# Performance work log

Measured on AMD Instinct MI355X. Metric: run time of the kernel, lower is better.

Reference implementation:

```python
import jax, jax.numpy as jnp
import numpy as np

N = 50000        # nodes
E = 600000       # edges
D = 128          # hidden dim
FID = 128        # fixed_input_dim (one-hot size)
RWSE = 16        # rwse_dim
G = 128          # num graphs
L = 4            # num GIN blocks
DEG = 1001       # degree embedding table (clamp to 1000)
GIN_EPS = 0.0
BN_EPS = 1e-5


def setup_inputs() -> dict:
    key = jax.random.key(0)
    ks = jax.random.split(key, 16)
    s = 0.05
    inp = {
        "feat_id": jax.random.randint(ks[0], (N,), 0, 100000),
        "edge_index": jax.random.randint(ks[1], (2, E), 0, N),
        "batch_idx": jnp.sort(jax.random.randint(ks[2], (N,), 0, G)),
        "rwse": jax.random.normal(ks[3], (N, RWSE), jnp.float32),
        "in_degrees": jax.random.randint(ks[4], (N,), 0, DEG),
        # parameters
        "value_W": jax.random.normal(ks[5], (FID, D), jnp.float32) * s,
        "value_b": jnp.zeros((D,), jnp.float32),
        "rwse_W": jax.random.normal(ks[6], (RWSE, D), jnp.float32) * s,
        "rwse_b": jnp.zeros((D,), jnp.float32),
        "deg_emb": jax.random.normal(ks[7], (DEG, D), jnp.float32) * s,
        "mlp_W1": jax.random.normal(ks[8], (L, D, D), jnp.float32) * s,
        "mlp_b1": jnp.zeros((L, D), jnp.float32),
        "mlp_W2": jax.random.normal(ks[9], (L, D, D), jnp.float32) * s,
        "mlp_b2": jnp.zeros((L, D), jnp.float32),
        "bn_gamma": 1.0 + jax.random.normal(ks[10], (L, D), jnp.float32) * s,
        "bn_beta": jax.random.normal(ks[11], (L, D), jnp.float32) * s,
        "bn_mean": jax.random.normal(ks[12], (L, D), jnp.float32) * s,
        "bn_var": 1.0 + jax.random.uniform(ks[13], (L, D), jnp.float32) * 0.1,
    }
    return inp


def reference(feat_id, edge_index, batch_idx, rwse, in_degrees,
              value_W, value_b, rwse_W, rwse_b, deg_emb,
              mlp_W1, mlp_b1, mlp_W2, mlp_b2,
              bn_gamma, bn_beta, bn_mean, bn_var):
    # one_hot(feat_id % FID) @ value_W  ==  row gather of value_W
    h_id = jnp.remainder(feat_id, FID)
    h_attr = value_W[h_id] + value_b                      # [N, D]
    h_attr = h_attr + rwse @ rwse_W + rwse_b              # rwse projection
    deg = jnp.clip(in_degrees, 0, DEG - 1)
    h = h_attr + deg_emb[deg]                             # [N, D]

    src, dst = edge_index[0], edge_index[1]
    for l in range(L):
        # GIN aggregation: sum of neighbor messages + (1+eps)*self
        agg = jax.ops.segment_sum(h[src], dst, num_segments=N)
        agg = agg + (1.0 + GIN_EPS) * h
        # MLP: Linear -> ReLU -> Linear
        m = jax.nn.relu(agg @ mlp_W1[l] + mlp_b1[l]) @ mlp_W2[l] + mlp_b2[l]
        # BatchNorm (inference stats) + ReLU
        inv = bn_gamma[l] * jax.lax.rsqrt(bn_var[l] + BN_EPS)
        h = jax.nn.relu((m - bn_mean[l]) * inv + bn_beta[l])

    # scatter-mean graph pooling
    pooled = jax.ops.segment_sum(h, batch_idx, num_segments=G)      # [G, D]
    count = jax.ops.segment_sum(jnp.ones((N, 1), h.dtype), batch_idx,
                                num_segments=G)                     # [G, 1]
    graph_feature = pooled / jnp.maximum(count, 1.0)
    return graph_feature, h
```

## Files before the change

kernel.cpp:

```cpp
#include <hip/hip_runtime.h>

#define N_NODES 50000
#define N_EDGES 600000
#define DIM 128
#define NGRAPH 128
#define NLAYER 4
#define BN_EPS 1e-5f
#define SCAN_BLK 1024

using short8  = __attribute__((ext_vector_type(8))) short;
using float4v = __attribute__((ext_vector_type(4))) float;

__device__ __forceinline__ float bf2f(unsigned short u) {
    union { unsigned int i; float f; } c; c.i = ((unsigned int)u) << 16; return c.f;
}
__device__ __forceinline__ unsigned short f2bf(float f) {
    union { float f; unsigned int i; } c; c.f = f;
    unsigned int x = c.i;
    return (unsigned short)((x + 0x7fffu + ((x >> 16) & 1u)) >> 16);
}

__global__ void encode_kernel(const int* __restrict__ feat_id,
                              const float* __restrict__ rwse,
                              const int* __restrict__ indeg,
                              const float* __restrict__ value_W,
                              const float* __restrict__ value_b,
                              const float* __restrict__ rwse_W,
                              const float* __restrict__ rwse_b,
                              const float* __restrict__ deg_emb,
                              unsigned short* __restrict__ hout)
{
    int idx = blockIdx.x * blockDim.x + threadIdx.x;
    if (idx >= N_NODES * DIM) return;
    int n = idx >> 7, d = idx & 127;
    int fid = feat_id[n] & 127;
    float v = value_W[fid * DIM + d] + value_b[d] + rwse_b[d];
    const float* rr = rwse + n * 16;
    float acc = 0.f;
#pragma unroll
    for (int k = 0; k < 16; ++k) acc += rr[k] * rwse_W[k * DIM + d];
    v += acc;
    int dg = indeg[n]; dg = dg < 0 ? 0 : (dg > 1000 ? 1000 : dg);
    v += deg_emb[dg * DIM + d];
    hout[idx] = f2bf(v);
}

__global__ void hist_kernel(const int* __restrict__ dst, int* __restrict__ cnt) {
    int e = blockIdx.x * blockDim.x + threadIdx.x;
    if (e < N_EDGES) atomicAdd(&cnt[dst[e]], 1);
}

__global__ void scanA_kernel(const int* __restrict__ cnt, int* __restrict__ rp, int* __restrict__ bsum) {
    __shared__ int sc[SCAN_BLK];
    int t = threadIdx.x, i = blockIdx.x * SCAN_BLK + t;
    int v = (i < N_NODES) ? cnt[i] : 0;
    sc[t] = v; __syncthreads();
    for (int off = 1; off < SCAN_BLK; off <<= 1) {
        int add = (t >= off) ? sc[t - off] : 0;
        __syncthreads();
        sc[t] += add;
        __syncthreads();
    }
    if (i < N_NODES) rp[i] = sc[t] - v;
    if (t == SCAN_BLK - 1) bsum[blockIdx.x] = sc[t];
}

__global__ void scanB_kernel(const int* __restrict__ bsum, int* __restrict__ bsx, int nb) {
    int lane = threadIdx.x;
    int v = (lane < nb) ? bsum[lane] : 0;
    int orig = v;
    for (int off = 1; off < 64; off <<= 1) {
        int y = __shfl_up(v, off, 64);
        if (lane >= off) v += y;
    }
    if (lane < nb) bsx[lane] = v - orig;
}

__global__ void scanC_kernel(int* __restrict__ rp, const int* __restrict__ bsx, int* __restrict__ cur) {
    int i = blockIdx.x * blockDim.x + threadIdx.x;
    if (i < N_NODES) { int v = rp[i] + bsx[i >> 10]; rp[i] = v; cur[i] = v; }
    else if (i == N_NODES) rp[i] = N_EDGES;
}

__global__ void scatter_kernel(const int* __restrict__ src, const int* __restrict__ dst,
                               int* __restrict__ cur, int* __restrict__ esrc) {
    int e = blockIdx.x * blockDim.x + threadIdx.x;
    if (e < N_EDGES) {
        int pos = atomicAdd(&cur[dst[e]], 1);
        esrc[pos] = src[e];
    }
}

__global__ void wtrans_kernel(const float* __restrict__ W1, const float* __restrict__ W2,
                              unsigned short* __restrict__ w1t, unsigned short* __restrict__ w2t) {
    int idx = blockIdx.x * blockDim.x + threadIdx.x;
    if (idx >= 2 * NLAYER * DIM * DIM) return;
    int i = idx & (DIM * DIM - 1);
    int l = (idx >> 14) & 3;
    int is2 = idx >= NLAYER * DIM * DIM;
    int n = i >> 7, k = i & 127;
    const float* W = (is2 ? W2 : W1) + l * DIM * DIM;
    unsigned short v = f2bf(W[k * DIM + n]);
    (is2 ? w2t : w1t)[l * DIM * DIM + n * DIM + k] = v;
}

__global__ void __launch_bounds__(256) agg_kernel(const unsigned short* __restrict__ hin,
                                                  const int* __restrict__ rp,
                                                  const int* __restrict__ esrc,
                                                  unsigned short* __restrict__ aggout)
{
    int node = (blockIdx.x * blockDim.x + threadIdx.x) >> 6;
    if (node >= N_NODES) return;
    int lane = threadIdx.x & 63;
    int grp = lane >> 4, q = lane & 15;

    float a[8];
    if (grp == 0) {
        uint4 s = *(const uint4*)(hin + (size_t)node * DIM + q * 8);
        a[0] = bf2f((unsigned short)(s.x & 0xffff)); a[1] = bf2f((unsigned short)(s.x >> 16));
        a[2] = bf2f((unsigned short)(s.y & 0xffff)); a[3] = bf2f((unsigned short)(s.y >> 16));
        a[4] = bf2f((unsigned short)(s.z & 0xffff)); a[5] = bf2f((unsigned short)(s.z >> 16));
        a[6] = bf2f((unsigned short)(s.w & 0xffff)); a[7] = bf2f((unsigned short)(s.w >> 16));
    } else {
#pragma unroll
        for (int i = 0; i < 8; ++i) a[i] = 0.f;
    }

    int e1 = rp[node + 1];
    for (int e = rp[node] + grp; e < e1; e += 4) {
        int s = esrc[e];
        uint4 v = *(const uint4*)(hin + (size_t)s * DIM + q * 8);
        a[0] += bf2f((unsigned short)(v.x & 0xffff)); a[1] += bf2f((unsigned short)(v.x >> 16));
        a[2] += bf2f((unsigned short)(v.y & 0xffff)); a[3] += bf2f((unsigned short)(v.y >> 16));
        a[4] += bf2f((unsigned short)(v.z & 0xffff)); a[5] += bf2f((unsigned short)(v.z >> 16));
        a[6] += bf2f((unsigned short)(v.w & 0xffff)); a[7] += bf2f((unsigned short)(v.w >> 16));
    }

#pragma unroll
    for (int i = 0; i < 8; ++i) {
        a[i] += __shfl_xor(a[i], 16, 64);
        a[i] += __shfl_xor(a[i], 32, 64);
    }

    if (grp == 0) {
        uint4 o;
        o.x = (unsigned int)f2bf(a[0]) | ((unsigned int)f2bf(a[1]) << 16);
        o.y = (unsigned int)f2bf(a[2]) | ((unsigned int)f2bf(a[3]) << 16);
        o.z = (unsigned int)f2bf(a[4]) | ((unsigned int)f2bf(a[5]) << 16);
        o.w = (unsigned int)f2bf(a[6]) | ((unsigned int)f2bf(a[7]) << 16);
        *(uint4*)(aggout + (size_t)node * DIM + q * 8) = o;
    }
}

__global__ void __launch_bounds__(256, 2) mlp_kernel(
    const unsigned short* __restrict__ aggin,
    const unsigned short* __restrict__ w1t,
    const unsigned short* __restrict__ w2t,
    const float* __restrict__ b1, const float* __restrict__ b2,
    const float* __restrict__ gam, const float* __restrict__ bet,
    const float* __restrict__ mean, const float* __restrict__ var,
    unsigned short* __restrict__ hout, float* __restrict__ fout, int last)
{
    __shared__ unsigned short sA[DIM * DIM];
    __shared__ unsigned short sW[DIM * DIM];
    const int tid = threadIdx.x;
    const int wave = tid >> 6, lane = tid & 63;
    const int fr = lane & 15, fg = lane >> 4;
    const int rowbase = blockIdx.x * DIM;

    for (int i = tid * 8; i < DIM * DIM; i += 256 * 8) {
        short8 v = *(const short8*)(w1t + i);
        int n = i >> 7;
        int byte = i * 2; byte ^= (n & 7) << 4;
        *(short8*)((char*)sW + byte) = v;
    }
    for (int i = tid * 8; i < DIM * DIM; i += 256 * 8) {
        int row = i >> 7;
        int node = rowbase + row;
        short8 v;
        if (node < N_NODES) v = *(const short8*)(aggin + (size_t)node * DIM + (i & 127));
        else { short z = 0; v = (short8){z,z,z,z,z,z,z,z}; }
        int byte = i * 2; byte ^= (row & 7) << 4;
        *(short8*)((char*)sA + byte) = v;
    }
    __syncthreads();

    float4v acc[2][8];
#pragma unroll
    for (int m = 0; m < 2; ++m)
#pragma unroll
        for (int n = 0; n < 8; ++n) acc[m][n] = (float4v){0.f, 0.f, 0.f, 0.f};

#pragma unroll
    for (int ks = 0; ks < 4; ++ks) {
        int k0 = ks * 32 + fg * 8;
        short8 a0, a1;
        { int row = wave * 32 + fr;      int byte = row * 256 + k0 * 2; byte ^= (row & 7) << 4; a0 = *(const short8*)((char*)sA + byte); }
        { int row = wave * 32 + 16 + fr; int byte = row * 256 + k0 * 2; byte ^= (row & 7) << 4; a1 = *(const short8*)((char*)sA + byte); }
#pragma unroll
        for (int nb = 0; nb < 8; ++nb) {
            int col = nb * 16 + fr;
            int byte = col * 256 + k0 * 2; byte ^= (col & 7) << 4;
            short8 b = *(const short8*)((char*)sW + byte);
            acc[0][nb] = __builtin_amdgcn_mfma_f32_16x16x32_bf16(a0, b, acc[0][nb], 0, 0, 0);
            acc[1][nb] = __builtin_amdgcn_mfma_f32_16x16x32_bf16(a1, b, acc[1][nb], 0, 0, 0);
        }
    }
    __syncthreads();

#pragma unroll
    for (int nb = 0; nb < 8; ++nb) {
        int col = nb * 16 + fr;
        float bias = b1[col];
#pragma unroll
        for (int m = 0; m < 2; ++m)
#pragma unroll
            for (int r = 0; r < 4; ++r) {
                int row = wave * 32 + m * 16 + fg * 4 + r;
                float v = acc[m][nb][r] + bias;
                v = fmaxf(v, 0.f);
                int byte = row * 256 + col * 2; byte ^= (row & 7) << 4;
                *(unsigned short*)((char*)sA + byte) = f2bf(v);
            }
    }
    for (int i = tid * 8; i < DIM * DIM; i += 256 * 8) {
        short8 v = *(const short8*)(w2t + i);
        int n = i >> 7;
        int byte = i * 2; byte ^= (n & 7) << 4;
        *(short8*)((char*)sW + byte) = v;
    }
    __syncthreads();

    float4v acc2[2][8];
#pragma unroll
    for (int m = 0; m < 2; ++m)
#pragma unroll
        for (int n = 0; n < 8; ++n) acc2[m][n] = (float4v){0.f, 0.f, 0.f, 0.f};

#pragma unroll
    for (int ks = 0; ks < 4; ++ks) {
        int k0 = ks * 32 + fg * 8;
        short8 a0, a1;
        { int row = wave * 32 + fr;      int byte = row * 256 + k0 * 2; byte ^= (row & 7) << 4; a0 = *(const short8*)((char*)sA + byte); }
        { int row = wave * 32 + 16 + fr; int byte = row * 256 + k0 * 2; byte ^= (row & 7) << 4; a1 = *(const short8*)((char*)sA + byte); }
#pragma unroll
        for (int nb = 0; nb < 8; ++nb) {
            int col = nb * 16 + fr;
            int byte = col * 256 + k0 * 2; byte ^= (col & 7) << 4;
            short8 b = *(const short8*)((char*)sW + byte);
            acc2[0][nb] = __builtin_amdgcn_mfma_f32_16x16x32_bf16(a0, b, acc2[0][nb], 0, 0, 0);
            acc2[1][nb] = __builtin_amdgcn_mfma_f32_16x16x32_bf16(a1, b, acc2[1][nb], 0, 0, 0);
        }
    }

#pragma unroll
    for (int nb = 0; nb < 8; ++nb) {
        int col = nb * 16 + fr;
        float bias = b2[col];
        float iv = gam[col] * rsqrtf(var[col] + BN_EPS);
        float mn = mean[col], bt = bet[col];
#pragma unroll
        for (int m = 0; m < 2; ++m)
#pragma unroll
            for (int r = 0; r < 4; ++r) {
                int row = wave * 32 + m * 16 + fg * 4 + r;
                int node = rowbase + row;
                if (node < N_NODES) {
                    float v = acc2[m][nb][r] + bias;
                    v = (v - mn) * iv + bt;
                    v = fmaxf(v, 0.f);
                    if (last) fout[(size_t)node * DIM + col] = v;
                    else hout[(size_t)node * DIM + col] = f2bf(v);
                }
            }
    }
}

__global__ void __launch_bounds__(256) pool_partial_kernel(const float* __restrict__ h,
                                                           const int* __restrict__ batch,
                                                           float* __restrict__ out)
{
    __shared__ float sums[256];
    __shared__ int sb[2];
    int g = blockIdx.x >> 3, split = blockIdx.x & 7;
    if (threadIdx.x < 2) {
        int target = g + threadIdx.x;
        int lo = 0, hi = N_NODES;
        while (lo < hi) { int mid = (lo + hi) >> 1; if (batch[mid] < target) lo = mid + 1; else hi = mid; }
        sb[threadIdx.x] = lo;
    }
    __syncthreads();
    int lo = sb[0], hi = sb[1];
    int d = threadIdx.x & 127, half = threadIdx.x >> 7;
    float acc = 0.f;
    for (int n = lo + split * 2 + half; n < hi; n += 16) acc += h[(size_t)n * DIM + d];
    sums[threadIdx.x] = acc;
    __syncthreads();
    if (threadIdx.x < 128) {
        float s = sums[threadIdx.x] + sums[threadIdx.x + 128];
        atomicAdd(&out[g * DIM + threadIdx.x], s);
    }
}

__global__ void pool_div_kernel(const int* __restrict__ batch, float* __restrict__ out)
{
    __shared__ int sb[2];
    int g = blockIdx.x;
    if (threadIdx.x < 2) {
        int target = g + threadIdx.x;
        int lo = 0, hi = N_NODES;
        while (lo < hi) { int mid = (lo + hi) >> 1; if (batch[mid] < target) lo = mid + 1; else hi = mid; }
        sb[threadIdx.x] = lo;
    }
    __syncthreads();
    float c = (float)(sb[1] - sb[0]);
    out[g * DIM + threadIdx.x] /= fmaxf(c, 1.f);
}

extern "C" void kernel_launch(void* const* d_in, const int* in_sizes, int n_in,
                              void* d_out, int out_size, void* d_ws, size_t ws_size,
                              hipStream_t stream)
{
    const int*   feat_id = (const int*)d_in[0];
    const int*   eidx    = (const int*)d_in[1];
    const int*   batch   = (const int*)d_in[2];
    const float* rwse    = (const float*)d_in[3];
    const int*   indeg   = (const int*)d_in[4];
    const float* value_W = (const float*)d_in[5];
    const float* value_b = (const float*)d_in[6];
    const float* rwse_W  = (const float*)d_in[7];
    const float* rwse_b  = (const float*)d_in[8];
    const float* deg_emb = (const float*)d_in[9];
    const float* W1      = (const float*)d_in[10];
    const float* b1      = (const float*)d_in[11];
    const float* W2      = (const float*)d_in[12];
    const float* b2      = (const float*)d_in[13];
    const float* gam     = (const float*)d_in[14];
    const float* bet     = (const float*)d_in[15];
    const float* mean    = (const float*)d_in[16];
    const float* var     = (const float*)d_in[17];

    const int* srcv = eidx;
    const int* dstv = eidx + N_EDGES;

    char* p = (char*)d_ws;
    auto alloc = [&](size_t bytes) { char* r = p; p += (bytes + 255) & ~(size_t)255; return r; };
    unsigned short* hA   = (unsigned short*)alloc((size_t)N_NODES * DIM * 2);
    unsigned short* agg  = (unsigned short*)alloc((size_t)N_NODES * DIM * 2);
    int* cnt  = (int*)alloc((size_t)N_NODES * 4);
    int* rp   = (int*)alloc((size_t)(N_NODES + 1) * 4);
    int* cur  = (int*)alloc((size_t)N_NODES * 4);
    int* bsum = (int*)alloc(64 * 4);
    int* bsx  = (int*)alloc(64 * 4);
    int* esrc = (int*)alloc((size_t)N_EDGES * 4);
    unsigned short* w1t = (unsigned short*)alloc((size_t)NLAYER * DIM * DIM * 2);
    unsigned short* w2t = (unsigned short*)alloc((size_t)NLAYER * DIM * DIM * 2);

    float* out = (float*)d_out;
    float* hf  = out + NGRAPH * DIM;

    hipMemsetAsync(cnt, 0, (size_t)N_NODES * 4, stream);
    hipMemsetAsync(out, 0, (size_t)NGRAPH * DIM * 4, stream);
    encode_kernel<<<(N_NODES * DIM + 255) / 256, 256, 0, stream>>>(
        feat_id, rwse, indeg, value_W, value_b, rwse_W, rwse_b, deg_emb, hA);
    hist_kernel<<<(N_EDGES + 255) / 256, 256, 0, stream>>>(dstv, cnt);
    int nsb = (N_NODES + SCAN_BLK - 1) / SCAN_BLK;
    scanA_kernel<<<nsb, SCAN_BLK, 0, stream>>>(cnt, rp, bsum);
    scanB_kernel<<<1, 64, 0, stream>>>(bsum, bsx, nsb);
    scanC_kernel<<<(N_NODES + 256) / 256, 256, 0, stream>>>(rp, bsx, cur);
    scatter_kernel<<<(N_EDGES + 255) / 256, 256, 0, stream>>>(srcv, dstv, cur, esrc);
    wtrans_kernel<<<(2 * NLAYER * DIM * DIM + 255) / 256, 256, 0, stream>>>(W1, W2, w1t, w2t);

    const int nrb = (N_NODES + DIM - 1) / DIM;
    for (int l = 0; l < NLAYER; ++l) {
        agg_kernel<<<(N_NODES * 64 + 255) / 256, 256, 0, stream>>>(hA, rp, esrc, agg);
        mlp_kernel<<<nrb, 256, 0, stream>>>(agg,
            w1t + l * DIM * DIM, w2t + l * DIM * DIM,
            b1 + l * DIM, b2 + l * DIM, gam + l * DIM, bet + l * DIM,
            mean + l * DIM, var + l * DIM,
            hA, hf, (l == NLAYER - 1) ? 1 : 0);
    }
    pool_partial_kernel<<<NGRAPH * 8, 256, 0, stream>>>(hf, batch, out);
    pool_div_kernel<<<NGRAPH, DIM, 0, stream>>>(batch, out);
}
```

Before: 437.9 us.

## Fuse preprocessing launches, halve MLP row tile, prefetch edges, drop pooling atomics

Merges encoding, weight transposition and degree histogram into one kernel, and the two scan fixup kernels into one, to cut launch overhead. The MLP kernel now processes 64 rows per block with higher occupancy bounds, to put more blocks across the CUs at the cost of reloading weights more often. The aggregation loop prefetches the next edge source index and makes the node index wave-uniform. Pooling writes per-split partials and combines them in a second kernel instead of using atomics and a memset.

```diff
diff --git a/kernel.cpp b/kernel.cpp
--- a/kernel.cpp
+++ b/kernel.cpp
@@ -7,6 +7,11 @@
 #define NLAYER 4
 #define BN_EPS 1e-5f
 #define SCAN_BLK 1024
+#define MROWS 64
+
+#define EN_BLOCKS 25000
+#define WT_BLOCKS 512
+#define HB_BLOCKS 2344
 
 using short8  = __attribute__((ext_vector_type(8))) short;
 using float4v = __attribute__((ext_vector_type(4))) float;
@@ -20,34 +25,49 @@
     return (unsigned short)((x + 0x7fffu + ((x >> 16) & 1u)) >> 16);
 }
 
-__global__ void encode_kernel(const int* __restrict__ feat_id,
-                              const float* __restrict__ rwse,
-                              const int* __restrict__ indeg,
-                              const float* __restrict__ value_W,
-                              const float* __restrict__ value_b,
-                              const float* __restrict__ rwse_W,
-                              const float* __restrict__ rwse_b,
-                              const float* __restrict__ deg_emb,
-                              unsigned short* __restrict__ hout)
-{
-    int idx = blockIdx.x * blockDim.x + threadIdx.x;
-    if (idx >= N_NODES * DIM) return;
-    int n = idx >> 7, d = idx & 127;
-    int fid = feat_id[n] & 127;
-    float v = value_W[fid * DIM + d] + value_b[d] + rwse_b[d];
-    const float* rr = rwse + n * 16;
-    float acc = 0.f;
-#pragma unroll
-    for (int k = 0; k < 16; ++k) acc += rr[k] * rwse_W[k * DIM + d];
-    v += acc;
-    int dg = indeg[n]; dg = dg < 0 ? 0 : (dg > 1000 ? 1000 : dg);
-    v += deg_emb[dg * DIM + d];
-    hout[idx] = f2bf(v);
-}
-
-__global__ void hist_kernel(const int* __restrict__ dst, int* __restrict__ cnt) {
-    int e = blockIdx.x * blockDim.x + threadIdx.x;
-    if (e < N_EDGES) atomicAdd(&cnt[dst[e]], 1);
+__global__ void fused_pre_kernel(const int* __restrict__ feat_id,
+                                 const float* __restrict__ rwse,
+                                 const int* __restrict__ indeg,
+                                 const float* __restrict__ value_W,
+                                 const float* __restrict__ value_b,
+                                 const float* __restrict__ rwse_W,
+                                 const float* __restrict__ rwse_b,
+                                 const float* __restrict__ deg_emb,
+                                 unsigned short* __restrict__ hout,
+                                 const float* __restrict__ W1,
+                                 const float* __restrict__ W2,
+                                 unsigned short* __restrict__ w1t,
+                                 unsigned short* __restrict__ w2t,
+                                 const int* __restrict__ dst,
+                                 int* __restrict__ cnt)
+{
+    int b = blockIdx.x;
+    if (b < EN_BLOCKS) {
+        int idx = b * 256 + threadIdx.x;
+        int n = idx >> 7, d = idx & 127;
+        int fid = feat_id[n] & 127;
+        float v = value_W[fid * DIM + d] + value_b[d] + rwse_b[d];
+        const float* rr = rwse + n * 16;
+        float acc = 0.f;
+#pragma unroll
+        for (int k = 0; k < 16; ++k) acc += rr[k] * rwse_W[k * DIM + d];
+        v += acc;
+        int dg = indeg[n]; dg = dg < 0 ? 0 : (dg > 1000 ? 1000 : dg);
+        v += deg_emb[dg * DIM + d];
+        hout[idx] = f2bf(v);
+    } else if (b < EN_BLOCKS + WT_BLOCKS) {
+        int idx = (b - EN_BLOCKS) * 256 + threadIdx.x;
+        int i = idx & (DIM * DIM - 1);
+        int l = (idx >> 14) & 3;
+        int is2 = idx >= NLAYER * DIM * DIM;
+        int n = i >> 7, k = i & 127;
+        const float* W = (is2 ? W2 : W1) + l * DIM * DIM;
+        unsigned short v = f2bf(W[k * DIM + n]);
+        (is2 ? w2t : w1t)[l * DIM * DIM + n * DIM + k] = v;
+    } else {
+        int e = (b - EN_BLOCKS - WT_BLOCKS) * 256 + threadIdx.x;
+        if (e < N_EDGES) atomicAdd(&cnt[dst[e]], 1);
+    }
 }
 
 __global__ void scanA_kernel(const int* __restrict__ cnt, int* __restrict__ rp, int* __restrict__ bsum) {
@@ -65,20 +85,22 @@
     if (t == SCAN_BLK - 1) bsum[blockIdx.x] = sc[t];
 }
 
-__global__ void scanB_kernel(const int* __restrict__ bsum, int* __restrict__ bsx, int nb) {
-    int lane = threadIdx.x;
-    int v = (lane < nb) ? bsum[lane] : 0;
-    int orig = v;
-    for (int off = 1; off < 64; off <<= 1) {
-        int y = __shfl_up(v, off, 64);
-        if (lane >= off) v += y;
-    }
-    if (lane < nb) bsx[lane] = v - orig;
-}
-
-__global__ void scanC_kernel(int* __restrict__ rp, const int* __restrict__ bsx, int* __restrict__ cur) {
-    int i = blockIdx.x * blockDim.x + threadIdx.x;
-    if (i < N_NODES) { int v = rp[i] + bsx[i >> 10]; rp[i] = v; cur[i] = v; }
+__global__ void scan_fixup_kernel(int* __restrict__ rp, const int* __restrict__ bsum,
+                                  int* __restrict__ cur, int nsb) {
+    __shared__ int sbx[64];
+    int t = threadIdx.x;
+    if (t < 64) {
+        int v = (t < nsb) ? bsum[t] : 0;
+        int orig = v;
+        for (int off = 1; off < 64; off <<= 1) {
+            int y = __shfl_up(v, off, 64);
+            if (t >= off) v += y;
+        }
+        sbx[t] = v - orig;
+    }
+    __syncthreads();
+    int i = blockIdx.x * 256 + t;
+    if (i < N_NODES) { int v = rp[i] + sbx[i >> 10]; rp[i] = v; cur[i] = v; }
     else if (i == N_NODES) rp[i] = N_EDGES;
 }
 
@@ -91,25 +113,13 @@
     }
 }
 
-__global__ void wtrans_kernel(const float* __restrict__ W1, const float* __restrict__ W2,
-                              unsigned short* __restrict__ w1t, unsigned short* __restrict__ w2t) {
-    int idx = blockIdx.x * blockDim.x + threadIdx.x;
-    if (idx >= 2 * NLAYER * DIM * DIM) return;
-    int i = idx & (DIM * DIM - 1);
-    int l = (idx >> 14) & 3;
-    int is2 = idx >= NLAYER * DIM * DIM;
-    int n = i >> 7, k = i & 127;
-    const float* W = (is2 ? W2 : W1) + l * DIM * DIM;
-    unsigned short v = f2bf(W[k * DIM + n]);
-    (is2 ? w2t : w1t)[l * DIM * DIM + n * DIM + k] = v;
-}
-
 __global__ void __launch_bounds__(256) agg_kernel(const unsigned short* __restrict__ hin,
                                                   const int* __restrict__ rp,
                                                   const int* __restrict__ esrc,
                                                   unsigned short* __restrict__ aggout)
 {
     int node = (blockIdx.x * blockDim.x + threadIdx.x) >> 6;
+    node = __builtin_amdgcn_readfirstlane(node);
     if (node >= N_NODES) return;
     int lane = threadIdx.x & 63;
     int grp = lane >> 4, q = lane & 15;
@@ -127,13 +137,18 @@
     }
 
     int e1 = rp[node + 1];
-    for (int e = rp[node] + grp; e < e1; e += 4) {
-        int s = esrc[e];
+    int e = rp[node] + grp;
+    int snext = (e < e1) ? esrc[e] : 0;
+    while (e < e1) {
+        int s = snext;
+        int en = e + 4;
+        snext = (en < e1) ? esrc[en] : 0;
         uint4 v = *(const uint4*)(hin + (size_t)s * DIM + q * 8);
         a[0] += bf2f((unsigned short)(v.x & 0xffff)); a[1] += bf2f((unsigned short)(v.x >> 16));
         a[2] += bf2f((unsigned short)(v.y & 0xffff)); a[3] += bf2f((unsigned short)(v.y >> 16));
         a[4] += bf2f((unsigned short)(v.z & 0xffff)); a[5] += bf2f((unsigned short)(v.z >> 16));
         a[6] += bf2f((unsigned short)(v.w & 0xffff)); a[7] += bf2f((unsigned short)(v.w >> 16));
+        e = en;
     }
 
 #pragma unroll
@@ -152,7 +167,7 @@
     }
 }
 
-__global__ void __launch_bounds__(256, 2) mlp_kernel(
+__global__ void __launch_bounds__(256, 3) mlp_kernel(
     const unsigned short* __restrict__ aggin,
     const unsigned short* __restrict__ w1t,
     const unsigned short* __restrict__ w2t,
@@ -161,12 +176,12 @@
     const float* __restrict__ mean, const float* __restrict__ var,
     unsigned short* __restrict__ hout, float* __restrict__ fout, int last)
 {
-    __shared__ unsigned short sA[DIM * DIM];
+    __shared__ unsigned short sA[MROWS * DIM];
     __shared__ unsigned short sW[DIM * DIM];
     const int tid = threadIdx.x;
     const int wave = tid >> 6, lane = tid & 63;
     const int fr = lane & 15, fg = lane >> 4;
-    const int rowbase = blockIdx.x * DIM;
+    const int rowbase = blockIdx.x * MROWS;
 
     for (int i = tid * 8; i < DIM * DIM; i += 256 * 8) {
         short8 v = *(const short8*)(w1t + i);
@@ -174,7 +189,7 @@
         int byte = i * 2; byte ^= (n & 7) << 4;
         *(short8*)((char*)sW + byte) = v;
     }
-    for (int i = tid * 8; i < DIM * DIM; i += 256 * 8) {
+    for (int i = tid * 8; i < MROWS * DIM; i += 256 * 8) {
         int row = i >> 7;
         int node = rowbase + row;
         short8 v;
@@ -185,25 +200,21 @@
     }
     __syncthreads();
 
-    float4v acc[2][8];
-#pragma unroll
-    for (int m = 0; m < 2; ++m)
-#pragma unroll
-        for (int n = 0; n < 8; ++n) acc[m][n] = (float4v){0.f, 0.f, 0.f, 0.f};
+    float4v acc[8];
+#pragma unroll
+    for (int n = 0; n < 8; ++n) acc[n] = (float4v){0.f, 0.f, 0.f, 0.f};
 
 #pragma unroll
     for (int ks = 0; ks < 4; ++ks) {
         int k0 = ks * 32 + fg * 8;
-        short8 a0, a1;
-        { int row = wave * 32 + fr;      int byte = row * 256 + k0 * 2; byte ^= (row & 7) << 4; a0 = *(const short8*)((char*)sA + byte); }
-        { int row = wave * 32 + 16 + fr; int byte = row * 256 + k0 * 2; byte ^= (row & 7) << 4; a1 = *(const short8*)((char*)sA + byte); }
+        short8 a0;
+        { int row = wave * 16 + fr; int byte = row * 256 + k0 * 2; byte ^= (row & 7) << 4; a0 = *(const short8*)((char*)sA + byte); }
 #pragma unroll
         for (int nb = 0; nb < 8; ++nb) {
             int col = nb * 16 + fr;
             int byte = col * 256 + k0 * 2; byte ^= (col & 7) << 4;
             short8 b = *(const short8*)((char*)sW + byte);
-            acc[0][nb] = __builtin_amdgcn_mfma_f32_16x16x32_bf16(a0, b, acc[0][nb], 0, 0, 0);
-            acc[1][nb] = __builtin_amdgcn_mfma_f32_16x16x32_bf16(a1, b, acc[1][nb], 0, 0, 0);
+            acc[nb] = __builtin_amdgcn_mfma_f32_16x16x32_bf16(a0, b, acc[nb], 0, 0, 0);
         }
     }
     __syncthreads();
@@ -213,15 +224,13 @@
         int col = nb * 16 + fr;
         float bias = b1[col];
 #pragma unroll
-        for (int m = 0; m < 2; ++m)
-#pragma unroll
-            for (int r = 0; r < 4; ++r) {
-                int row = wave * 32 + m * 16 + fg * 4 + r;
-                float v = acc[m][nb][r] + bias;
-                v = fmaxf(v, 0.f);
-                int byte = row * 256 + col * 2; byte ^= (row & 7) << 4;
-                *(unsigned short*)((char*)sA + byte) = f2bf(v);
-            }
+        for (int r = 0; r < 4; ++r) {
+            int row = wave * 16 + fg * 4 + r;
+            float v = acc[nb][r] + bias;
+            v = fmaxf(v, 0.f);
+            int byte = row * 256 + col * 2; byte ^= (row & 7) << 4;
+            *(unsigned short*)((char*)sA + byte) = f2bf(v);
+        }
     }
     for (int i = tid * 8; i < DIM * DIM; i += 256 * 8) {
         short8 v = *(const short8*)(w2t + i);
@@ -231,25 +240,21 @@
     }
     __syncthreads();
 
-    float4v acc2[2][8];
-#pragma unroll
-    for (int m = 0; m < 2; ++m)
-#pragma unroll
-        for (int n = 0; n < 8; ++n) acc2[m][n] = (float4v){0.f, 0.f, 0.f, 0.f};
+    float4v acc2[8];
+#pragma unroll
+    for (int n = 0; n < 8; ++n) acc2[n] = (float4v){0.f, 0.f, 0.f, 0.f};
 
 #pragma unroll
     for (int ks = 0; ks < 4; ++ks) {
         int k0 = ks * 32 + fg * 8;
-        short8 a0, a1;
-        { int row = wave * 32 + fr;      int byte = row * 256 + k0 * 2; byte ^= (row & 7) << 4; a0 = *(const short8*)((char*)sA + byte); }
-        { int row = wave * 32 + 16 + fr; int byte = row * 256 + k0 * 2; byte ^= (row & 7) << 4; a1 = *(const short8*)((char*)sA + byte); }
+        short8 a0;
+        { int row = wave * 16 + fr; int byte = row * 256 + k0 * 2; byte ^= (row & 7) << 4; a0 = *(const short8*)((char*)sA + byte); }
 #pragma unroll
         for (int nb = 0; nb < 8; ++nb) {
             int col = nb * 16 + fr;
             int byte = col * 256 + k0 * 2; byte ^= (col & 7) << 4;
             short8 b = *(const short8*)((char*)sW + byte);
-            acc2[0][nb] = __builtin_amdgcn_mfma_f32_16x16x32_bf16(a0, b, acc2[0][nb], 0, 0, 0);
-            acc2[1][nb] = __builtin_amdgcn_mfma_f32_16x16x32_bf16(a1, b, acc2[1][nb], 0, 0, 0);
+            acc2[nb] = __builtin_amdgcn_mfma_f32_16x16x32_bf16(a0, b, acc2[nb], 0, 0, 0);
         }
     }
 
@@ -260,25 +265,23 @@
         float iv = gam[col] * rsqrtf(var[col] + BN_EPS);
         float mn = mean[col], bt = bet[col];
 #pragma unroll
-        for (int m = 0; m < 2; ++m)
-#pragma unroll
-            for (int r = 0; r < 4; ++r) {
-                int row = wave * 32 + m * 16 + fg * 4 + r;
-                int node = rowbase + row;
-                if (node < N_NODES) {
-                    float v = acc2[m][nb][r] + bias;
-                    v = (v - mn) * iv + bt;
-                    v = fmaxf(v, 0.f);
-                    if (last) fout[(size_t)node * DIM + col] = v;
-                    else hout[(size_t)node * DIM + col] = f2bf(v);
-                }
+        for (int r = 0; r < 4; ++r) {
+            int row = wave * 16 + fg * 4 + r;
+            int node = rowbase + row;
+            if (node < N_NODES) {
+                float v = acc2[nb][r] + bias;
+                v = (v - mn) * iv + bt;
+                v = fmaxf(v, 0.f);
+                if (last) fout[(size_t)node * DIM + col] = v;
+                else hout[(size_t)node * DIM + col] = f2bf(v);
             }
+        }
     }
 }
 
 __global__ void __launch_bounds__(256) pool_partial_kernel(const float* __restrict__ h,
                                                            const int* __restrict__ batch,
-                                                           float* __restrict__ out)
+                                                           float* __restrict__ partial)
 {
     __shared__ float sums[256];
     __shared__ int sb[2];
@@ -296,25 +299,28 @@
     for (int n = lo + split * 2 + half; n < hi; n += 16) acc += h[(size_t)n * DIM + d];
     sums[threadIdx.x] = acc;
     __syncthreads();
-    if (threadIdx.x < 128) {
-        float s = sums[threadIdx.x] + sums[threadIdx.x + 128];
-        atomicAdd(&out[g * DIM + threadIdx.x], s);
-    }
-}
-
-__global__ void pool_div_kernel(const int* __restrict__ batch, float* __restrict__ out)
+    if (threadIdx.x < 128)
+        partial[blockIdx.x * DIM + threadIdx.x] = sums[threadIdx.x] + sums[threadIdx.x + 128];
+}
+
+__global__ void pool_comb_kernel(const float* __restrict__ partial,
+                                 const int* __restrict__ batch,
+                                 float* __restrict__ out)
 {
     __shared__ int sb[2];
-    int g = blockIdx.x;
-    if (threadIdx.x < 2) {
-        int target = g + threadIdx.x;
+    int g = blockIdx.x, t = threadIdx.x;
+    if (t < 2) {
+        int target = g + t;
         int lo = 0, hi = N_NODES;
         while (lo < hi) { int mid = (lo + hi) >> 1; if (batch[mid] < target) lo = mid + 1; else hi = mid; }
-        sb[threadIdx.x] = lo;
-    }
-    __syncthreads();
+        sb[t] = lo;
+    }
+    __syncthreads();
+    float s = 0.f;
+#pragma unroll
+    for (int sp = 0; sp < 8; ++sp) s += partial[(g * 8 + sp) * DIM + t];
     float c = (float)(sb[1] - sb[0]);
-    out[g * DIM + threadIdx.x] /= fmaxf(c, 1.f);
+    out[g * DIM + t] = s / fmaxf(c, 1.f);
 }
 
 extern "C" void kernel_launch(void* const* d_in, const int* in_sizes, int n_in,
@@ -351,27 +357,24 @@
     int* rp   = (int*)alloc((size_t)(N_NODES + 1) * 4);
     int* cur  = (int*)alloc((size_t)N_NODES * 4);
     int* bsum = (int*)alloc(64 * 4);
-    int* bsx  = (int*)alloc(64 * 4);
     int* esrc = (int*)alloc((size_t)N_EDGES * 4);
     unsigned short* w1t = (unsigned short*)alloc((size_t)NLAYER * DIM * DIM * 2);
     unsigned short* w2t = (unsigned short*)alloc((size_t)NLAYER * DIM * DIM * 2);
+    float* partial = (float*)alloc((size_t)NGRAPH * 8 * DIM * 4);
 
     float* out = (float*)d_out;
     float* hf  = out + NGRAPH * DIM;
 
     hipMemsetAsync(cnt, 0, (size_t)N_NODES * 4, stream);
-    hipMemsetAsync(out, 0, (size_t)NGRAPH * DIM * 4, stream);
-    encode_kernel<<<(N_NODES * DIM + 255) / 256, 256, 0, stream>>>(
-        feat_id, rwse, indeg, value_W, value_b, rwse_W, rwse_b, deg_emb, hA);
-    hist_kernel<<<(N_EDGES + 255) / 256, 256, 0, stream>>>(dstv, cnt);
+    fused_pre_kernel<<<EN_BLOCKS + WT_BLOCKS + HB_BLOCKS, 256, 0, stream>>>(
+        feat_id, rwse, indeg, value_W, value_b, rwse_W, rwse_b, deg_emb, hA,
+        W1, W2, w1t, w2t, dstv, cnt);
     int nsb = (N_NODES + SCAN_BLK - 1) / SCAN_BLK;
     scanA_kernel<<<nsb, SCAN_BLK, 0, stream>>>(cnt, rp, bsum);
-    scanB_kernel<<<1, 64, 0, stream>>>(bsum, bsx, nsb);
-    scanC_kernel<<<(N_NODES + 256) / 256, 256, 0, stream>>>(rp, bsx, cur);
+    scan_fixup_kernel<<<(N_NODES + 1 + 255) / 256, 256, 0, stream>>>(rp, bsum, cur, nsb);
     scatter_kernel<<<(N_EDGES + 255) / 256, 256, 0, stream>>>(srcv, dstv, cur, esrc);
-    wtrans_kernel<<<(2 * NLAYER * DIM * DIM + 255) / 256, 256, 0, stream>>>(W1, W2, w1t, w2t);
-
-    const int nrb = (N_NODES + DIM - 1) / DIM;
+
+    const int nrb = (N_NODES + MROWS - 1) / MROWS;
     for (int l = 0; l < NLAYER; ++l) {
         agg_kernel<<<(N_NODES * 64 + 255) / 256, 256, 0, stream>>>(hA, rp, esrc, agg);
         mlp_kernel<<<nrb, 256, 0, stream>>>(agg,
@@ -380,6 +383,6 @@
             mean + l * DIM, var + l * DIM,
             hA, hf, (l == NLAYER - 1) ? 1 : 0);
     }
-    pool_partial_kernel<<<NGRAPH * 8, 256, 0, stream>>>(hf, batch, out);
-    pool_div_kernel<<<NGRAPH, DIM, 0, stream>>>(batch, out);
-}
+    pool_partial_kernel<<<NGRAPH * 8, 256, 0, stream>>>(hf, batch, partial);
+    pool_comb_kernel<<<NGRAPH, DIM, 0, stream>>>(partial, batch, out);
+}
```

Result: no change. 432.0 us (-1.3%).
